# Performance work log

Hardware: AMD Instinct MI355X
Metric: run time of the kernel (lower is better)

The kernel has to match this reference:

```python
import jax, jax.numpy as jnp
import numpy as np

V, S, D, NL, DF, R, DG = 50257, 1024, 640, 16, 2560, 24, 256
PLU = R * (R - 1) // 2  # 276
OFFSETS = (1, 2, 4, 8, 16, 32, 64)
EPS = 1e-6
LN_EPS = 1e-5
II, JJ = np.triu_indices(R, k=1)  # matches torch.triu_indices(r, r, offset=1) ordering


def setup_inputs() -> dict:
    key = jax.random.key(0)
    ks = jax.random.split(key, 16)
    B, L = 4, 1024
    def n(k, shape):
        return jax.random.normal(k, shape, jnp.float32) * 0.02
    return {
        "input_ids": jax.random.randint(ks[0], (B, L), 0, V, jnp.int32),
        "tok_emb": n(ks[1], (V, D)),          # tied with lm_head
        "pos_emb": n(ks[2], (S, D)),
        "ln1_w": jnp.ones((NL, D)), "ln1_b": jnp.zeros((NL, D)),
        "red_w": n(ks[3], (NL, R, D)), "red_b": jnp.zeros((NL, R)),
        "gp1_w": n(ks[4], (NL, DG, PLU)), "gp1_b": jnp.zeros((NL, DG)),
        "gp2_w": n(ks[5], (NL, D, DG)), "gp2_b": jnp.zeros((NL, D)),
        "gate_w": n(ks[6], (NL, D, 2 * D)), "gate_b": jnp.zeros((NL, D)),
        "ln2_w": jnp.ones((NL, D)), "ln2_b": jnp.zeros((NL, D)),
        "fc1_w": n(ks[7], (NL, DF, D)), "fc1_b": jnp.zeros((NL, DF)),
        "fc2_w": n(ks[8], (NL, D, DF)), "fc2_b": jnp.zeros((NL, D)),
        "fn_w": jnp.ones((D,)), "fn_b": jnp.zeros((D,)),
    }


def _ln(x, w, b):
    m = jnp.mean(x, -1, keepdims=True)
    v = jnp.mean((x - m) ** 2, -1, keepdims=True)
    return (x - m) / jnp.sqrt(v + LN_EPS) * w + b


def _forward(input_ids, tok_emb, pos_emb, ln1_w, ln1_b, red_w, red_b,
             gp1_w, gp1_b, gp2_w, gp2_b, gate_w, gate_b,
             ln2_w, ln2_b, fc1_w, fc1_b, fc2_w, fc2_b, fn_w, fn_b):
    B, L = input_ids.shape
    x = tok_emb[input_ids] + pos_emb[jnp.arange(L)][None]  # (B,L,D), dropout=0 (eval)
    for l in range(NL):
        # --- CausalGrassmannMixer ---
        h = _ln(x, ln1_w[l], ln1_b[l])
        z = jnp.einsum('bld,rd->blr', h, red_w[l]) + red_b[l]  # (B,L,R)
        geom_sum = jnp.zeros_like(h)
        count = jnp.zeros((B, L, 1), h.dtype)
        for delta in OFFSETS:
            if delta >= L:
                continue
            z_past = jnp.pad(z[:, :L - delta], ((0, 0), (delta, 0), (0, 0)))
            # Plucker coordinates, normalized
            p = z_past[..., II] * z[..., JJ] - z_past[..., JJ] * z[..., II]  # (B,L,PLU)
            norm = jnp.maximum(jnp.sqrt(jnp.sum(p * p, -1, keepdims=True)), EPS)
            p = p / norm
            g = jax.nn.gelu(jnp.einsum('blp,gp->blg', p, gp1_w[l]) + gp1_b[l], approximate=False)
            g = jnp.einsum('blg,dg->bld', g, gp2_w[l]) + gp2_b[l]
            mask = (jnp.arange(L) >= delta).astype(h.dtype)[None, :, None]
            geom_sum = geom_sum + g * mask
            count = count + mask
        g = geom_sum / jnp.maximum(count, 1.0)
        alpha = jax.nn.sigmoid(
            jnp.einsum('ble,de->bld', jnp.concatenate([h, g], -1), gate_w[l]) + gate_b[l])
        x = x + alpha * h + (1.0 - alpha) * g
        # --- FeedForward ---
        h2 = _ln(x, ln2_w[l], ln2_b[l])
        ff = jax.nn.gelu(jnp.einsum('bld,fd->blf', h2, fc1_w[l]) + fc1_b[l], approximate=False)
        x = x + jnp.einsum('blf,df->bld', ff, fc2_w[l]) + fc2_b[l]
    x = _ln(x, fn_w, fn_b)
    return jnp.einsum('bld,vd->blv', x, tok_emb)  # tied lm_head


def reference(input_ids, tok_emb, pos_emb, ln1_w, ln1_b, red_w, red_b,
              gp1_w, gp1_b, gp2_w, gp2_b, gate_w, gate_b,
              ln2_w, ln2_b, fc1_w, fc1_b, fc2_w, fc2_b, fn_w, fn_b):
    return _forward(input_ids, tok_emb, pos_emb, ln1_w, ln1_b, red_w, red_b,
                    gp1_w, gp1_b, gp2_w, gp2_b, gate_w, gate_b,
                    ln2_w, ln2_b, fc1_w, fc1_b, fc2_w, fc2_b, fn_w, fn_b)
```

## Files before the change

kernel.cpp:

```cpp
#include <hip/hip_runtime.h>
#include <cmath>

#define V_ 50257
#define D_ 640
#define NL_ 16
#define DF_ 2560
#define R_ 24
#define DG_ 256
#define PLU_ 276
#define PLUP_ 288
#define B_ 4
#define L_ 1024
#define M_ (B_*L_)
#define EPS_ 1e-6f
#define LN_EPS_ 1e-5f

typedef __bf16 bf16x8 __attribute__((ext_vector_type(8)));
typedef float f32x4 __attribute__((ext_vector_type(4)));

__device__ __forceinline__ float gelu_exact(float x) {
    return 0.5f * x * (1.0f + erff(x * 0.70710678118654752f));
}
__device__ __forceinline__ float sigmoid_f(float x) {
    return 1.0f / (1.0f + expf(-x));
}
__device__ __forceinline__ ushort f2b(float f) {
    union { float f; unsigned u; } v; v.f = f;
    unsigned u = v.u;
    return (ushort)((u + 0x7FFFu + ((u >> 16) & 1u)) >> 16);
}
__device__ __forceinline__ float b2f(ushort b) {
    union { unsigned u; float f; } v; v.u = ((unsigned)b) << 16;
    return v.f;
}

#define GLOAD16(gptr, lptr) \
    __builtin_amdgcn_global_load_lds((const __attribute__((address_space(1))) void*)(gptr), \
                                     (__attribute__((address_space(3))) void*)(lptr), 16, 0, 0)


#define AS_(b) (shmem + (b) * 4096)
#define BS_(b) (shmem + 8192 + (b) * 4096)
#define STAGE128(b, k0) do { \
    GLOAD16(A + (size_t)(bm + w * 32 + srow) * (size_t)K + ((k0) + scol), AS_(b) + (w * 32) * 32); \
    GLOAD16(A + (size_t)(bm + w * 32 + 16 + srow) * (size_t)K + ((k0) + scol), AS_(b) + (w * 32 + 16) * 32); \
    int rb0_ = bn + w * 32 + srow;      if (rb0_ > N - 1) rb0_ = N - 1; \
    int rb1_ = bn + w * 32 + 16 + srow; if (rb1_ > N - 1) rb1_ = N - 1; \
    GLOAD16(W + (size_t)rb0_ * (size_t)K + ((k0) + scol), BS_(b) + (w * 32) * 32); \
    GLOAD16(W + (size_t)rb1_ * (size_t)K + ((k0) + scol), BS_(b) + (w * 32 + 16) * 32); \
} while (0)

template<int EPI>
__global__ __launch_bounds__(256) void mgemm128_k(
    const ushort* __restrict__ A, const ushort* __restrict__ W,
    const float* __restrict__ bias, float* __restrict__ Cf,
    ushort* __restrict__ Cb, int M, int N, int K)
{
    __shared__ ushort shmem[16384];
    const int tid = threadIdx.x;
    const int lane = tid & 63;
    const int w = tid >> 6;
    const int wr = w >> 1, wc = w & 1;
    const int lr = lane & 15, lk = lane >> 4;
    const int bm = blockIdx.x * 128, bn = blockIdx.y * 128;
    const int srow = lane >> 2;
    const int scol = (((lane & 3) ^ ((srow >> 1) & 3)) * 8);

    f32x4 acc[4][4] = {};
    const int nt = K >> 5;

    STAGE128(0, 0);
    asm volatile("s_waitcnt vmcnt(0)" ::: "memory");
    __builtin_amdgcn_s_barrier();

    int cur = 0;
    for (int t = 0; t < nt; ++t) {
        if (t + 1 < nt) { STAGE128(cur ^ 1, (t + 1) * 32); }
        bf16x8 af[4], bfr[4];
        #pragma unroll
        for (int m = 0; m < 4; ++m) {
            int rr = wr * 64 + m * 16 + lr;
            af[m] = *reinterpret_cast<const bf16x8*>(&AS_(cur)[rr * 32 + ((lk ^ ((rr >> 1) & 3)) * 8)]);
        }
        #pragma unroll
        for (int n = 0; n < 4; ++n) {
            int rr = wc * 64 + n * 16 + lr;
            bfr[n] = *reinterpret_cast<const bf16x8*>(&BS_(cur)[rr * 32 + ((lk ^ ((rr >> 1) & 3)) * 8)]);
        }
        #pragma unroll
        for (int m = 0; m < 4; ++m)
            #pragma unroll
            for (int n = 0; n < 4; ++n)
                acc[m][n] = __builtin_amdgcn_mfma_f32_16x16x32_bf16(af[m], bfr[n], acc[m][n], 0, 0, 0);
        asm volatile("s_waitcnt vmcnt(0)" ::: "memory");
        __builtin_amdgcn_s_barrier();
        cur ^= 1;
    }

    #pragma unroll
    for (int n = 0; n < 4; ++n) {
        int col = bn + wc * 64 + n * 16 + lr;
        if (col >= N) continue;
        float bsv = bias ? bias[col] : 0.0f;
        #pragma unroll
        for (int m = 0; m < 4; ++m) {
            #pragma unroll
            for (int r4 = 0; r4 < 4; ++r4) {
                int row = bm + wr * 64 + m * 16 + lk * 4 + r4;
                float o = acc[m][n][r4] + bsv;
                size_t idx = (size_t)row * N + col;
                if (EPI == 1) Cb[idx] = f2b(gelu_exact(o));
                else          Cb[idx] = f2b(o);
            }
        }
    }
}

#define AS2_(b) (shmem + (b) * 8192)
#define BS2_(b) (shmem + 16384 + (b) * 4096)
#define STAGE256(b, k0) do { \
    GLOAD16(A + (size_t)(bm + w * 32 + srow) * (size_t)K + ((k0) + scol), AS2_(b) + (w * 32) * 32); \
    GLOAD16(A + (size_t)(bm + w * 32 + 16 + srow) * (size_t)K + ((k0) + scol), AS2_(b) + (w * 32 + 16) * 32); \
    int rb_ = bn + w * 16 + srow; if (rb_ > N - 1) rb_ = N - 1; \
    GLOAD16(W + (size_t)rb_ * (size_t)K + ((k0) + scol), BS2_(b) + (w * 16) * 32); \
} while (0)

__global__ __launch_bounds__(512) void mgemm256nt_k(
    const ushort* __restrict__ A, const ushort* __restrict__ W,
    float* __restrict__ Cf, int M, int N, int K)
{
    __shared__ ushort shmem[24576];
    const int tid = threadIdx.x;
    const int lane = tid & 63;
    const int w = tid >> 6;
    const int wr = w >> 1, wc = w & 1;
    const int lr = lane & 15, lk = lane >> 4;
    const int bm = blockIdx.x * 256, bn = blockIdx.y * 128;
    const int srow = lane >> 2;
    const int scol = (((lane & 3) ^ ((srow >> 1) & 3)) * 8);

    f32x4 acc[4][4] = {};
    const int nt = K >> 5;

    STAGE256(0, 0);
    asm volatile("s_waitcnt vmcnt(0)" ::: "memory");
    __builtin_amdgcn_s_barrier();

    int cur = 0;
    for (int t = 0; t < nt; ++t) {
        if (t + 1 < nt) { STAGE256(cur ^ 1, (t + 1) * 32); }
        bf16x8 af[4], bfr[4];
        #pragma unroll
        for (int m = 0; m < 4; ++m) {
            int rr = wr * 64 + m * 16 + lr;
            af[m] = *reinterpret_cast<const bf16x8*>(&AS2_(cur)[rr * 32 + ((lk ^ ((rr >> 1) & 3)) * 8)]);
        }
        #pragma unroll
        for (int n = 0; n < 4; ++n) {
            int rr = wc * 64 + n * 16 + lr;
            bfr[n] = *reinterpret_cast<const bf16x8*>(&BS2_(cur)[rr * 32 + ((lk ^ ((rr >> 1) & 3)) * 8)]);
        }
        #pragma unroll
        for (int m = 0; m < 4; ++m)
            #pragma unroll
            for (int n = 0; n < 4; ++n)
                acc[m][n] = __builtin_amdgcn_mfma_f32_16x16x32_bf16(af[m], bfr[n], acc[m][n], 0, 0, 0);
        asm volatile("s_waitcnt vmcnt(0)" ::: "memory");
        __builtin_amdgcn_s_barrier();
        cur ^= 1;
    }

    float* lds_f = (float*)shmem;
    const int wbase = w * (16 * 68);
    #pragma unroll
    for (int m = 0; m < 4; ++m) {
        #pragma unroll
        for (int n = 0; n < 4; ++n) {
            #pragma unroll
            for (int r4 = 0; r4 < 4; ++r4)
                lds_f[wbase + (lk * 4 + r4) * 68 + n * 16 + lr] = acc[m][n][r4];
        }
        __syncthreads();
        #pragma unroll
        for (int r = 0; r < 16; ++r) {
            int row = bm + wr * 64 + m * 16 + r;
            int col = bn + wc * 64 + lane;
            float v = lds_f[wbase + r * 68 + lane];
            if (col < N)
                __builtin_nontemporal_store(v, &Cf[(size_t)row * N + col]);
        }
        __syncthreads();
    }
}

#define STAGE12864(b, k0) do { \
    GLOAD16(A + (size_t)(bm + w * 16 + srow) * (size_t)K + ((k0) + scol), &As[b][(w * 16) * 32]); \
    GLOAD16(A + (size_t)(bm + 64 + w * 16 + srow) * (size_t)K + ((k0) + scol), &As[b][(64 + w * 16) * 32]); \
    GLOAD16(W + (size_t)(bn + w * 16 + srow) * (size_t)K + ((k0) + scol), &Bs[b][(w * 16) * 32]); \
} while (0)

template<int EPI>
__global__ __launch_bounds__(256) void mgemm12864_k(
    const ushort* __restrict__ A, const ushort* __restrict__ W,
    const float* __restrict__ bias, float* __restrict__ Cf,
    const ushort* __restrict__ hg, ushort* __restrict__ ub,
    int M, int N, int K)
{
    __shared__ ushort As[2][128 * 32];
    __shared__ ushort Bs[2][64 * 32];
    const int tid = threadIdx.x;
    const int lane = tid & 63;
    const int w = tid >> 6;
    const int wr = w >> 1, wc = w & 1;
    const int lr = lane & 15, lk = lane >> 4;
    const int bm = blockIdx.x * 128, bn = blockIdx.y * 64;
    const int srow = lane >> 2;
    const int scol = (((lane & 3) ^ ((srow >> 1) & 3)) * 8);

    f32x4 acc[4][2] = {};
    const int nt = K >> 5;

    STAGE12864(0, 0);
    asm volatile("s_waitcnt vmcnt(0)" ::: "memory");
    __builtin_amdgcn_s_barrier();

    int cur = 0;
    for (int t = 0; t < nt; ++t) {
        if (t + 1 < nt) { STAGE12864(cur ^ 1, (t + 1) * 32); }
        bf16x8 af[4], bfr[2];
        #pragma unroll
        for (int m = 0; m < 4; ++m) {
            int rr = wr * 64 + m * 16 + lr;
            af[m] = *reinterpret_cast<const bf16x8*>(&As[cur][rr * 32 + ((lk ^ ((rr >> 1) & 3)) * 8)]);
        }
        #pragma unroll
        for (int n = 0; n < 2; ++n) {
            int rr = wc * 32 + n * 16 + lr;
            bfr[n] = *reinterpret_cast<const bf16x8*>(&Bs[cur][rr * 32 + ((lk ^ ((rr >> 1) & 3)) * 8)]);
        }
        #pragma unroll
        for (int m = 0; m < 4; ++m)
            #pragma unroll
            for (int n = 0; n < 2; ++n)
                acc[m][n] = __builtin_amdgcn_mfma_f32_16x16x32_bf16(af[m], bfr[n], acc[m][n], 0, 0, 0);
        asm volatile("s_waitcnt vmcnt(0)" ::: "memory");
        __builtin_amdgcn_s_barrier();
        cur ^= 1;
    }

    #pragma unroll
    for (int n = 0; n < 2; ++n) {
        int col = bn + wc * 32 + n * 16 + lr;
        float bsv = bias ? bias[col] : 0.0f;
        #pragma unroll
        for (int m = 0; m < 4; ++m) {
            #pragma unroll
            for (int r4 = 0; r4 < 4; ++r4) {
                int row = bm + wr * 64 + m * 16 + lk * 4 + r4;
                float o = acc[m][n][r4] + bsv;
                size_t idx = (size_t)row * N + col;
                if (EPI == 2) {
                    float a = sigmoid_f(o);
                    float hv = b2f(hg[(size_t)row * (2 * D_) + col]);
                    float gv = b2f(hg[(size_t)row * (2 * D_) + D_ + col]);
                    Cf[idx] = Cf[idx] + a * hv + (1.0f - a) * gv;
                } else if (EPI == 3) {
                    Cf[idx] += o;
                } else if (EPI == 5) {
                    if ((row & (L_ - 1)) == 0) o = 0.0f;
                    ub[(size_t)row * (2 * D_) + D_ + col] = f2b(o);
                }
            }
        }
    }
}

__global__ __launch_bounds__(256) void credsum_k(
    const ushort* __restrict__ c1b, ushort* __restrict__ crb)
{
    int idx4 = blockIdx.x * 256 + threadIdx.x;
    if (idx4 >= M_ * DG_ / 4) return;
    int idx = idx4 * 4;
    int row = idx / DG_;
    int l = row & (L_ - 1);
    float s0 = 0.f, s1 = 0.f, s2 = 0.f, s3 = 0.f;
    int c = 0;
    #pragma unroll
    for (int oi = 0; oi < 7; ++oi) {
        if (l >= (1 << oi)) {
            ushort4 v = *reinterpret_cast<const ushort4*>(c1b + (size_t)oi * M_ * DG_ + idx);
            s0 += b2f(v.x); s1 += b2f(v.y); s2 += b2f(v.z); s3 += b2f(v.w);
            ++c;
        }
    }
    float inv = 1.0f / (float)max(c, 1);
    ushort4 o;
    o.x = f2b(s0 * inv); o.y = f2b(s1 * inv); o.z = f2b(s2 * inv); o.w = f2b(s3 * inv);
    *reinterpret_cast<ushort4*>(crb + idx) = o;
}

__global__ __launch_bounds__(128) void lnred_k(
    const float* __restrict__ x, const float* __restrict__ w,
    const float* __restrict__ b, const float* __restrict__ rw,
    const float* __restrict__ rb, ushort* __restrict__ hgb,
    float* __restrict__ z)
{
    int row = blockIdx.x;
    int tid = threadIdx.x;
    const float* xr = x + (size_t)row * D_;
    __shared__ float hrow[D_];
    __shared__ float parts[R_][5];
    float v[5];
    float sum = 0.f, sumsq = 0.f;
    #pragma unroll
    for (int t = 0; t < 5; ++t) {
        v[t] = xr[tid + t * 128];
        sum += v[t]; sumsq += v[t] * v[t];
    }
    #pragma unroll
    for (int off = 32; off > 0; off >>= 1) {
        sum += __shfl_down(sum, off);
        sumsq += __shfl_down(sumsq, off);
    }
    __shared__ float s0[2], s1[2];
    if ((tid & 63) == 0) { s0[tid >> 6] = sum; s1[tid >> 6] = sumsq; }
    __syncthreads();
    float m = (s0[0] + s0[1]) * (1.0f / D_);
    float var = (s1[0] + s1[1]) * (1.0f / D_) - m * m;
    float inv = rsqrtf(var + LN_EPS_);
    #pragma unroll
    for (int t = 0; t < 5; ++t) {
        int d = tid + t * 128;
        float o = (v[t] - m) * inv * w[d] + b[d];
        hgb[(size_t)row * (2 * D_) + d] = f2b(o);
        hrow[d] = o;
    }
    __syncthreads();
    if (tid < 120) {
        int c = tid / 5, ch = tid - c * 5;
        const float4* hv = (const float4*)(hrow + ch * 128);
        const float4* wv = (const float4*)(rw + (size_t)c * D_ + ch * 128);
        float p = 0.f;
        #pragma unroll 8
        for (int k = 0; k < 32; ++k) {
            float4 a = hv[k], bb = wv[k];
            p += a.x * bb.x + a.y * bb.y + a.z * bb.z + a.w * bb.w;
        }
        parts[c][ch] = p;
    }
    __syncthreads();
    if (tid < R_) {
        float s = parts[tid][0] + parts[tid][1] + parts[tid][2] + parts[tid][3] + parts[tid][4];
        z[(size_t)row * R_ + tid] = s + rb[tid];
    }
}

__global__ __launch_bounds__(256) void embed_k(
    const int* __restrict__ ids, const float* __restrict__ tok,
    const float* __restrict__ pos, float* __restrict__ x)
{
    int idx = blockIdx.x * 256 + threadIdx.x;
    if (idx >= M_ * D_) return;
    int row = idx / D_;
    int d = idx - row * D_;
    int l = row & (L_ - 1);
    x[idx] = tok[(size_t)ids[row] * D_ + d] + pos[(size_t)l * D_ + d];
}

__global__ __launch_bounds__(256) void cvt_k(
    const float* __restrict__ src, ushort* __restrict__ dst, int n)
{
    int idx = blockIdx.x * 256 + threadIdx.x;
    if (idx < n) dst[idx] = f2b(src[idx]);
}

#define WC_G1  73728
#define WC_G2  (WC_G1 + 163840)
#define WC_GT  (WC_G2 + 819200)
#define WC_F1  (WC_GT + 1638400)
#define WC_F2  (WC_F1 + 1638400)
__device__ __forceinline__ void wconv_body(
    int idx, const float* g1, const float* g2, const float* gt,
    const float* f1, const float* f2, ushort* wb)
{
    if (idx < WC_G1) {
        int row = idx / PLUP_, c = idx - row * PLUP_;
        wb[idx] = (c < PLU_) ? f2b(g1[row * PLU_ + c]) : (ushort)0;
    } else if (idx < WC_G2) {
        wb[idx] = f2b(g2[idx - WC_G1]);
    } else if (idx < WC_GT) {
        wb[idx] = f2b(gt[idx - WC_G2]);
    } else if (idx < WC_F1) {
        wb[idx] = f2b(f1[idx - WC_GT]);
    } else if (idx < WC_F2) {
        wb[idx] = f2b(f2[idx - WC_F1]);
    }
}

__global__ __launch_bounds__(256) void wconv_k(
    const float* __restrict__ g1, const float* __restrict__ g2,
    const float* __restrict__ gt, const float* __restrict__ f1,
    const float* __restrict__ f2, ushort* __restrict__ wb)
{
    int idx = blockIdx.x * 256 + threadIdx.x;
    wconv_body(idx, g1, g2, gt, f1, f2, wb);
}

__global__ __launch_bounds__(256) void wconv_all_k(
    const float* __restrict__ g1, const float* __restrict__ g2,
    const float* __restrict__ gt, const float* __restrict__ f1,
    const float* __restrict__ f2, ushort* __restrict__ wb_all)
{
    int l = blockIdx.y;
    int idx = blockIdx.x * 256 + threadIdx.x;
    wconv_body(idx,
               g1 + (size_t)l * DG_ * PLU_, g2 + (size_t)l * D_ * DG_,
               gt + (size_t)l * D_ * 2 * D_, f1 + (size_t)l * DF_ * D_,
               f2 + (size_t)l * D_ * DF_, wb_all + (size_t)l * WC_F2);
}

__global__ __launch_bounds__(128) void ln_k(
    const float* __restrict__ x, const float* __restrict__ w,
    const float* __restrict__ b, float* __restrict__ outf,
    ushort* __restrict__ outb, int bstride)
{
    int row = blockIdx.x;
    int tid = threadIdx.x;
    const float* xr = x + (size_t)row * D_;
    float v[5];
    float sum = 0.f, sumsq = 0.f;
    #pragma unroll
    for (int t = 0; t < 5; ++t) {
        v[t] = xr[tid + t * 128];
        sum += v[t]; sumsq += v[t] * v[t];
    }
    #pragma unroll
    for (int off = 32; off > 0; off >>= 1) {
        sum += __shfl_down(sum, off);
        sumsq += __shfl_down(sumsq, off);
    }
    __shared__ float s0[2], s1[2];
    if ((tid & 63) == 0) { s0[tid >> 6] = sum; s1[tid >> 6] = sumsq; }
    __syncthreads();
    float m = (s0[0] + s0[1]) * (1.0f / D_);
    float var = (s1[0] + s1[1]) * (1.0f / D_) - m * m;
    float inv = rsqrtf(var + LN_EPS_);
    #pragma unroll
    for (int t = 0; t < 5; ++t) {
        int d = tid + t * 128;
        float o = (v[t] - m) * inv * w[d] + b[d];
        if (outf) outf[(size_t)row * D_ + d] = o;
        if (outb) outb[(size_t)row * bstride + d] = f2b(o);
    }
}

__global__ __launch_bounds__(128) void plucker7_k(
    const float* __restrict__ z, ushort* __restrict__ pb)
{
    int oi = blockIdx.y;
    int delta = 1 << oi;
    int row = blockIdx.x;
    int l = row & (L_ - 1);
    int tid = threadIdx.x;
    ushort* out = pb + ((size_t)oi * M_ + row) * PLUP_;
    if (l < delta) {
        for (int idx = tid; idx < PLUP_; idx += 128) out[idx] = 0;
        return;
    }
    __shared__ float zc[R_], zp[R_];
    if (tid < R_) {
        zc[tid] = z[(size_t)row * R_ + tid];
        zp[tid] = z[(size_t)(row - delta) * R_ + tid];
    }
    __syncthreads();
    float vals[3];
    float ss = 0.f;
    #pragma unroll
    for (int t = 0; t < 3; ++t) {
        int idx = tid + t * 128;
        float val = 0.f;
        if (idx < PLU_) {
            int i = 0, rem = idx;
            while (rem >= 23 - i) { rem -= 23 - i; ++i; }
            int j = i + 1 + rem;
            val = zp[i] * zc[j] - zp[j] * zc[i];
        }
        vals[t] = val;
        ss += val * val;
    }
    #pragma unroll
    for (int off = 32; off > 0; off >>= 1) ss += __shfl_down(ss, off);
    __shared__ float wsum[2];
    if ((tid & 63) == 0) wsum[tid >> 6] = ss;
    __syncthreads();
    float inv = 1.0f / fmaxf(sqrtf(wsum[0] + wsum[1]), EPS_);
    #pragma unroll
    for (int t = 0; t < 3; ++t) {
        int idx = tid + t * 128;
        if (idx < PLUP_) out[idx] = (idx < PLU_) ? f2b(vals[t] * inv) : (ushort)0;
    }
}

static void mg128(int epi, const ushort* A, const ushort* W, const float* bias,
                  float* Cf, ushort* Cb, int M, int N, int K, hipStream_t s)
{
    dim3 grid(M / 128, (N + 127) / 128), block(256);
    if (epi == 1) mgemm128_k<1><<<grid, block, 0, s>>>(A, W, bias, Cf, Cb, M, N, K);
    else          mgemm128_k<4><<<grid, block, 0, s>>>(A, W, bias, Cf, Cb, M, N, K);
}

static void mg12864(int epi, const ushort* A, const ushort* W, const float* bias,
                    float* Cf, const ushort* hg, ushort* ub,
                    int M, int N, int K, hipStream_t s)
{
    dim3 grid(M / 128, N / 64), block(256);
    if (epi == 2)      mgemm12864_k<2><<<grid, block, 0, s>>>(A, W, bias, Cf, hg, ub, M, N, K);
    else if (epi == 3) mgemm12864_k<3><<<grid, block, 0, s>>>(A, W, bias, Cf, hg, ub, M, N, K);
    else               mgemm12864_k<5><<<grid, block, 0, s>>>(A, W, bias, Cf, hg, ub, M, N, K);
}

extern "C" void kernel_launch(void* const* d_in, const int* in_sizes, int n_in,
                              void* d_out, int out_size, void* d_ws, size_t ws_size,
                              hipStream_t stream)
{
    const int*   ids   = (const int*)d_in[0];
    const float* tok   = (const float*)d_in[1];
    const float* pos   = (const float*)d_in[2];
    const float* ln1w  = (const float*)d_in[3];
    const float* ln1b  = (const float*)d_in[4];
    const float* redw  = (const float*)d_in[5];
    const float* redb  = (const float*)d_in[6];
    const float* gp1w  = (const float*)d_in[7];
    const float* gp1b  = (const float*)d_in[8];
    const float* gp2w  = (const float*)d_in[9];
    const float* gp2b  = (const float*)d_in[10];
    const float* gatew = (const float*)d_in[11];
    const float* gateb = (const float*)d_in[12];
    const float* ln2w  = (const float*)d_in[13];
    const float* ln2b  = (const float*)d_in[14];
    const float* fc1w  = (const float*)d_in[15];
    const float* fc1b  = (const float*)d_in[16];
    const float* fc2w  = (const float*)d_in[17];
    const float* fc2b  = (const float*)d_in[18];
    const float* fnw   = (const float*)d_in[19];
    const float* fnb   = (const float*)d_in[20];
    float* out = (float*)d_out;

    const size_t MD = (size_t)M_ * D_;
    float* ws = (float*)d_ws;
    float* x = ws;
    float* z = x + MD;
    ushort* pb    = (ushort*)(z + (size_t)M_ * R_);
    ushort* c1b   = pb + (size_t)7 * M_ * PLUP_;
    ushort* crb   = c1b + (size_t)7 * M_ * DG_;
    ushort* hgb   = crb + (size_t)M_ * DG_;
    ushort* h2b   = hgb + (size_t)M_ * 2 * D_;
    ushort* ffb   = h2b + MD;
    ushort* xnb   = ffb + (size_t)M_ * DF_;
    ushort* tokb  = xnb + MD;
    ushort* wb    = tokb + (size_t)V_ * D_;

    const size_t base_bytes = (size_t)((char*)wb - (char*)d_ws);
    const bool all_w = ws_size >= base_bytes + (size_t)NL_ * WC_F2 * 2;

    const int ELT_GRID = (M_ * D_ + 255) / 256;
    const int WC_GRID = (WC_F2 + 255) / 256;

    embed_k<<<ELT_GRID, 256, 0, stream>>>(ids, tok, pos, x);
    cvt_k<<<(V_ * D_ + 255) / 256, 256, 0, stream>>>(tok, tokb, V_ * D_);
    if (all_w)
        wconv_all_k<<<dim3(WC_GRID, NL_), 256, 0, stream>>>(gp1w, gp2w, gatew, fc1w, fc2w, wb);

    for (int l = 0; l < NL_; ++l) {
        const ushort* wbl = all_w ? wb + (size_t)l * WC_F2 : wb;
        if (!all_w)
            wconv_k<<<WC_GRID, 256, 0, stream>>>(
                gp1w + (size_t)l * DG_ * PLU_, gp2w + (size_t)l * D_ * DG_,
                gatew + (size_t)l * D_ * 2 * D_, fc1w + (size_t)l * DF_ * D_,
                fc2w + (size_t)l * D_ * DF_, wb);
        lnred_k<<<M_, 128, 0, stream>>>(x, ln1w + (size_t)l * D_, ln1b + (size_t)l * D_,
                                        redw + (size_t)l * R_ * D_, redb + (size_t)l * R_,
                                        hgb, z);
        plucker7_k<<<dim3(M_, 7), 128, 0, stream>>>(z, pb);
        mg128(1, pb, wbl, gp1b + (size_t)l * DG_, nullptr, c1b, 7 * M_, DG_, PLUP_, stream);
        credsum_k<<<(M_ * DG_ / 4 + 255) / 256, 256, 0, stream>>>(c1b, crb);
        mg12864(5, crb, wbl + WC_G1, gp2b + (size_t)l * D_, nullptr, hgb, hgb,
                M_, D_, DG_, stream);
        mg12864(2, hgb, wbl + WC_G2, gateb + (size_t)l * D_, x, hgb, nullptr,
                M_, D_, 2 * D_, stream);
        ln_k<<<M_, 128, 0, stream>>>(x, ln2w + (size_t)l * D_, ln2b + (size_t)l * D_,
                                     nullptr, h2b, D_);
        mg128(1, h2b, wbl + WC_GT, fc1b + (size_t)l * DF_, nullptr, ffb, M_, DF_, D_, stream);
        mg12864(3, ffb, wbl + WC_F1, fc2b + (size_t)l * D_, x, nullptr, nullptr,
                M_, D_, DF_, stream);
    }
    ln_k<<<M_, 128, 0, stream>>>(x, fnw, fnb, nullptr, xnb, D_);
    {
        dim3 grid(M_ / 256, (V_ + 127) / 128), block(512);
        mgemm256nt_k<<<grid, block, 0, stream>>>(xnb, tokb, out, M_, V_, D_);
    }
}
```

Measured before the change: 4.047 ms.

## Triple-buffer LDS staging in GEMM kernels with two tiles in flight

Converts the three bf16 MFMA GEMM kernels from double to triple-buffered LDS staging. Each loop now prefetches tile t+2 and waits with partial vmcnt counts, so one global load stays outstanding during compute instead of draining every iteration. This aims to hide global-load latency behind the MFMA work. In exchange it uses more LDS per block, which can lower occupancy, and it relies on the hand-set vmcnt counts matching the number of loads issued per stage.

```diff
diff --git a/kernel.cpp b/kernel.cpp
--- a/kernel.cpp
+++ b/kernel.cpp
@@ -39,8 +39,14 @@
                                      (__attribute__((address_space(3))) void*)(lptr), 16, 0, 0)
 
 
+#define PIPE_FENCE() do { \
+    asm volatile("s_waitcnt lgkmcnt(0)" ::: "memory"); \
+    __builtin_amdgcn_sched_barrier(0); \
+    __builtin_amdgcn_s_barrier(); \
+} while (0)
+
 #define AS_(b) (shmem + (b) * 4096)
-#define BS_(b) (shmem + 8192 + (b) * 4096)
+#define BS_(b) (shmem + 12288 + (b) * 4096)
 #define STAGE128(b, k0) do { \
     GLOAD16(A + (size_t)(bm + w * 32 + srow) * (size_t)K + ((k0) + scol), AS_(b) + (w * 32) * 32); \
     GLOAD16(A + (size_t)(bm + w * 32 + 16 + srow) * (size_t)K + ((k0) + scol), AS_(b) + (w * 32 + 16) * 32); \
@@ -56,7 +62,7 @@
     const float* __restrict__ bias, float* __restrict__ Cf,
     ushort* __restrict__ Cb, int M, int N, int K)
 {
-    __shared__ ushort shmem[16384];
+    __shared__ ushort shmem[24576];
     const int tid = threadIdx.x;
     const int lane = tid & 63;
     const int w = tid >> 6;
@@ -70,12 +76,20 @@
     const int nt = K >> 5;
 
     STAGE128(0, 0);
-    asm volatile("s_waitcnt vmcnt(0)" ::: "memory");
-    __builtin_amdgcn_s_barrier();
-
-    int cur = 0;
+    STAGE128(1, 32);
+
     for (int t = 0; t < nt; ++t) {
-        if (t + 1 < nt) { STAGE128(cur ^ 1, (t + 1) * 32); }
+        const int cur = t % 3;
+        if (t + 2 < nt) {
+            STAGE128((t + 2) % 3, (t + 2) * 32);
+            asm volatile("s_waitcnt vmcnt(8)" ::: "memory");
+        } else if (t + 1 < nt) {
+            asm volatile("s_waitcnt vmcnt(4)" ::: "memory");
+        } else {
+            asm volatile("s_waitcnt vmcnt(0)" ::: "memory");
+        }
+        __builtin_amdgcn_s_barrier();
+
         bf16x8 af[4], bfr[4];
         #pragma unroll
         for (int m = 0; m < 4; ++m) {
@@ -92,9 +106,7 @@
             #pragma unroll
             for (int n = 0; n < 4; ++n)
                 acc[m][n] = __builtin_amdgcn_mfma_f32_16x16x32_bf16(af[m], bfr[n], acc[m][n], 0, 0, 0);
-        asm volatile("s_waitcnt vmcnt(0)" ::: "memory");
-        __builtin_amdgcn_s_barrier();
-        cur ^= 1;
+        PIPE_FENCE();
     }
 
     #pragma unroll
@@ -117,7 +129,7 @@
 }
 
 #define AS2_(b) (shmem + (b) * 8192)
-#define BS2_(b) (shmem + 16384 + (b) * 4096)
+#define BS2_(b) (shmem + 24576 + (b) * 4096)
 #define STAGE256(b, k0) do { \
     GLOAD16(A + (size_t)(bm + w * 32 + srow) * (size_t)K + ((k0) + scol), AS2_(b) + (w * 32) * 32); \
     GLOAD16(A + (size_t)(bm + w * 32 + 16 + srow) * (size_t)K + ((k0) + scol), AS2_(b) + (w * 32 + 16) * 32); \
@@ -129,7 +141,7 @@
     const ushort* __restrict__ A, const ushort* __restrict__ W,
     float* __restrict__ Cf, int M, int N, int K)
 {
-    __shared__ ushort shmem[24576];
+    __shared__ ushort shmem[36864];
     const int tid = threadIdx.x;
     const int lane = tid & 63;
     const int w = tid >> 6;
@@ -143,12 +155,20 @@
     const int nt = K >> 5;
 
     STAGE256(0, 0);
-    asm volatile("s_waitcnt vmcnt(0)" ::: "memory");
-    __builtin_amdgcn_s_barrier();
-
-    int cur = 0;
+    STAGE256(1, 32);
+
     for (int t = 0; t < nt; ++t) {
-        if (t + 1 < nt) { STAGE256(cur ^ 1, (t + 1) * 32); }
+        const int cur = t % 3;
+        if (t + 2 < nt) {
+            STAGE256((t + 2) % 3, (t + 2) * 32);
+            asm volatile("s_waitcnt vmcnt(6)" ::: "memory");
+        } else if (t + 1 < nt) {
+            asm volatile("s_waitcnt vmcnt(3)" ::: "memory");
+        } else {
+            asm volatile("s_waitcnt vmcnt(0)" ::: "memory");
+        }
+        __builtin_amdgcn_s_barrier();
+
         bf16x8 af[4], bfr[4];
         #pragma unroll
         for (int m = 0; m < 4; ++m) {
@@ -165,9 +185,7 @@
             #pragma unroll
             for (int n = 0; n < 4; ++n)
                 acc[m][n] = __builtin_amdgcn_mfma_f32_16x16x32_bf16(af[m], bfr[n], acc[m][n], 0, 0, 0);
-        asm volatile("s_waitcnt vmcnt(0)" ::: "memory");
-        __builtin_amdgcn_s_barrier();
-        cur ^= 1;
+        PIPE_FENCE();
     }
 
     float* lds_f = (float*)shmem;
@@ -206,8 +224,8 @@
     const ushort* __restrict__ hg, ushort* __restrict__ ub,
     int M, int N, int K)
 {
-    __shared__ ushort As[2][128 * 32];
-    __shared__ ushort Bs[2][64 * 32];
+    __shared__ ushort As[3][128 * 32];
+    __shared__ ushort Bs[3][64 * 32];
     const int tid = threadIdx.x;
     const int lane = tid & 63;
     const int w = tid >> 6;
@@ -221,12 +239,20 @@
     const int nt = K >> 5;
 
     STAGE12864(0, 0);
-    asm volatile("s_waitcnt vmcnt(0)" ::: "memory");
-    __builtin_amdgcn_s_barrier();
-
-    int cur = 0;
+    STAGE12864(1, 32);
+
     for (int t = 0; t < nt; ++t) {
-        if (t + 1 < nt) { STAGE12864(cur ^ 1, (t + 1) * 32); }
+        const int cur = t % 3;
+        if (t + 2 < nt) {
+            STAGE12864((t + 2) % 3, (t + 2) * 32);
+            asm volatile("s_waitcnt vmcnt(6)" ::: "memory");
+        } else if (t + 1 < nt) {
+            asm volatile("s_waitcnt vmcnt(3)" ::: "memory");
+        } else {
+            asm volatile("s_waitcnt vmcnt(0)" ::: "memory");
+        }
+        __builtin_amdgcn_s_barrier();
+
         bf16x8 af[4], bfr[2];
         #pragma unroll
         for (int m = 0; m < 4; ++m) {
@@ -243,9 +269,7 @@
             #pragma unroll
             for (int n = 0; n < 2; ++n)
                 acc[m][n] = __builtin_amdgcn_mfma_f32_16x16x32_bf16(af[m], bfr[n], acc[m][n], 0, 0, 0);
-        asm volatile("s_waitcnt vmcnt(0)" ::: "memory");
-        __builtin_amdgcn_s_barrier();
-        cur ^= 1;
+        PIPE_FENCE();
     }
 
     #pragma unroll
```

New measurement: 4.189 ms. +3.5%, slower.
